# Kernel tuning notes

Measured on AMD Instinct MI355X. Metric: run time of the kernel, lower is better.

The kernel has to match this reference:

```python
import jax, jax.numpy as jnp
import numpy as np

# ---- static config (mirrors build() with the chosen init_kwargs) ----
B, H, W, C = 16, 56, 56, 128
KH, KW = 3, 3          # filter_size
SH, SW = 1, 1          # stride
NF = 256               # n_filters
IN_FEAT = C * KH * KW  # 1152
NNZ = int(1 * 0.2 * IN_FEAT * NF)  # multiple * density * n_parameters = 58982


def _make_indices():
    """Replicates the full='output' sparsity-pattern construction from build()."""
    rng = np.random.default_rng(0)
    per_col = NNZ // NF
    remain = NNZ % NF
    remain_cols = set(rng.choice(NF, remain, replace=False).tolist())
    chunks = []
    for col in rng.permutation(NF):
        k = per_col + (1 if int(col) in remain_cols else 0)
        rows = rng.choice(IN_FEAT, k, replace=False)
        chunks.append(np.stack([rows, np.full(k, col, dtype=np.int64)], axis=1))
    return np.concatenate(chunks, axis=0).astype(np.int32)  # (NNZ, 2) [row, col]


def setup_inputs() -> dict:
    key = jax.random.key(0)
    k1, k2 = jax.random.split(key)
    x = jax.random.normal(k1, (B, H, W, C), dtype=jnp.float32)
    limit = float(np.sqrt(6.0 / (IN_FEAT + NF)))  # glorot_uniform on the sparse values
    kernel = jax.random.uniform(k2, (NNZ,), jnp.float32, -limit, limit)
    bias = jnp.zeros((NF,), jnp.float32)
    indices = jnp.asarray(_make_indices())
    return {"x": x, "kernel": kernel, "bias": bias, "indices": indices}


def _im2col_valid(x):
    # tf.image.extract_patches ordering: patch positions row-major (di, dj),
    # channels fastest -> concatenate C-channel slices in (di, dj) order.
    oh = (H - KH) // SH + 1
    ow = (W - KW) // SW + 1
    cols = [x[:, di:di + oh * SH:SH, dj:dj + ow * SW:SW, :]
            for di in range(KH) for dj in range(KW)]
    return jnp.concatenate(cols, axis=-1), oh, ow  # (B, oh, ow, IN_FEAT)


def reference(x, kernel, bias, indices):
    patches, oh, ow = _im2col_valid(x)
    pm = patches.reshape(-1, IN_FEAT)  # (B*oh*ow, IN_FEAT)
    # Sparse (IN_FEAT, NF) weight: scatter values into a dense matrix
    # (indices are unique by construction, so .add == .set and is grad-safe).
    Wm = jnp.zeros((IN_FEAT, NF), dtype=pm.dtype).at[indices[:, 0], indices[:, 1]].add(kernel)
    out = pm @ Wm + bias            # sparse-dense matmul + bias
    out = jax.nn.relu(out)          # activation
    return out.reshape(B, oh, ow, NF)
```

## Files before the change

kernel.cpp:

```cpp
#include <hip/hip_runtime.h>

typedef unsigned short u16;
typedef __bf16 bf16x8 __attribute__((ext_vector_type(8)));
typedef float f32x4 __attribute__((ext_vector_type(4)));

#define B_   16
#define H_   56
#define W_   56
#define C_   128
#define OH_  54
#define OW_  54
#define NF_  256
#define KF_  1152
#define M_   46656
#define NNZ_ 58982

#define XB_ELEMS (B_*H_*W_*C_)
#define WT_ELEMS (KF_*NF_)

__device__ __forceinline__ u16 f2bf(float f) {
    unsigned u = __float_as_uint(f);
    u += 0x7FFFu + ((u >> 16) & 1u);
    return (u16)(u >> 16);
}

__device__ __forceinline__ void gload16(const void* g, void* l) {
    __builtin_amdgcn_global_load_lds(
        (const __attribute__((address_space(1))) unsigned int*)g,
        (__attribute__((address_space(3))) unsigned int*)l,
        16, 0, 0);
}

__global__ __launch_bounds__(256) void cvt_x_kernel(const float* __restrict__ x,
                                                    u16* __restrict__ xb,
                                                    u16* __restrict__ wt) {
    if (blockIdx.x < 144) {
        uint4 z = {0u, 0u, 0u, 0u};
        ((uint4*)wt)[blockIdx.x * 256 + threadIdx.x] = z;
    }
    int i = (blockIdx.x * 256 + threadIdx.x) * 8;
    float4 v0 = *(const float4*)(x + i);
    float4 v1 = *(const float4*)(x + i + 4);
    union { u16 u[8]; uint4 v; } r;
    r.u[0] = f2bf(v0.x); r.u[1] = f2bf(v0.y); r.u[2] = f2bf(v0.z); r.u[3] = f2bf(v0.w);
    r.u[4] = f2bf(v1.x); r.u[5] = f2bf(v1.y); r.u[6] = f2bf(v1.z); r.u[7] = f2bf(v1.w);
    *(uint4*)(xb + i) = r.v;
}

__global__ __launch_bounds__(256) void scatter_kernel(const float* __restrict__ kv,
                                                      const int* __restrict__ idx,
                                                      u16* __restrict__ wt) {
    int t = blockIdx.x * 256 + threadIdx.x;
    if (t >= NNZ_) return;
    int k   = idx[2*t];
    int col = idx[2*t + 1];
    wt[(k >> 3) * 2048 + col * 8 + (k & 7)] = f2bf(kv[t]);
}

__global__ __launch_bounds__(512, 2) void spconv_gemm(const u16* __restrict__ xb,
                                                      const u16* __restrict__ wt,
                                                      const float* __restrict__ bias,
                                                      float* __restrict__ out) {
    __shared__ __align__(16) u16 As[2][12288];
    __shared__ __align__(16) u16 Bs[2][16384];

    const int t    = threadIdx.x;
    const int l    = t & 63;
    const int w    = t >> 6;
    const int r16  = l & 15;
    const int ks   = l >> 4;
    const int wr   = w >> 2;
    const int wc   = w & 3;
    const int m0   = blockIdx.x * 192;

    const int r0  = t >> 3;
    const int sd  = t & 7;
    const int kco = (sd ^ (r0 & 7)) * 8;
    const u16* a_base[3];
#pragma unroll
    for (int j = 0; j < 3; ++j) {
        int mg  = m0 + r0 + j * 64;
        int bb  = mg / (OH_ * OW_);
        int rem = mg % (OH_ * OW_);
        int ii  = rem / OW_;
        int jj  = rem % OW_;
        a_base[j] = xb + ((bb * H_ + ii) * W_ + jj) * C_;
    }

    f32x4 acc[6][4];
    const f32x4 zz = {0.f, 0.f, 0.f, 0.f};
#pragma unroll
    for (int i = 0; i < 6; ++i)
#pragma unroll
        for (int j = 0; j < 4; ++j) acc[i][j] = zz;

#define ISSUE(kt, bi) do {                                                  \
    int g_  = (kt) >> 1;                                                    \
    int di_ = (g_ * 11) >> 5;                                               \
    int dj_ = g_ - 3 * di_;                                                 \
    int apix_ = (di_ * W_ + dj_) * C_ + ((kt) & 1) * 64 + kco;              \
    gload16(a_base[0] + apix_, &As[bi][t * 8]);                             \
    gload16(a_base[1] + apix_, &As[bi][t * 8 + 4096]);                      \
    gload16(a_base[2] + apix_, &As[bi][t * 8 + 8192]);                      \
    const u16* bsrc_ = wt + (kt) * 16384 + t * 8;                           \
    gload16(bsrc_,         &Bs[bi][t * 8]);                                 \
    gload16(bsrc_ + 4096,  &Bs[bi][t * 8 + 4096]);                          \
    gload16(bsrc_ + 8192,  &Bs[bi][t * 8 + 8192]);                          \
    gload16(bsrc_ + 12288, &Bs[bi][t * 8 + 12288]);                         \
} while (0)

#define COMPUTE(bi) do {                                                    \
    _Pragma("unroll")                                                       \
    for (int h = 0; h < 2; ++h) {                                           \
        const int chs_ = ((h * 4 + ks) ^ (r16 & 7)) * 8;                    \
        bf16x8 af_[6];                                                      \
        _Pragma("unroll")                                                   \
        for (int mf = 0; mf < 6; ++mf)                                      \
            af_[mf] = *(const bf16x8*)(&As[bi][(wr * 96 + mf * 16 + r16) * 64 + chs_]); \
        _Pragma("unroll")                                                   \
        for (int nf = 0; nf < 4; ++nf) {                                    \
            bf16x8 bf_ = *(const bf16x8*)(&Bs[bi][((h * 4 + ks) * 256 + wc * 64 + nf * 16 + r16) * 8]); \
            _Pragma("unroll")                                               \
            for (int mf = 0; mf < 6; ++mf)                                  \
                acc[mf][nf] = __builtin_amdgcn_mfma_f32_16x16x32_bf16(      \
                    af_[mf], bf_, acc[mf][nf], 0, 0, 0);                    \
        }                                                                   \
    }                                                                       \
} while (0)

#define WAITVM(n) asm volatile("s_waitcnt vmcnt(" #n ")" ::: "memory")
#define BAR() do { __builtin_amdgcn_s_barrier();                            \
                   asm volatile("" ::: "memory"); } while (0)

    ISSUE(0, 0);
    ISSUE(1, 1);

#pragma unroll
    for (int k = 0; k < 16; ++k) {
        WAITVM(7);
        BAR();
        COMPUTE(k & 1);
        BAR();
        ISSUE(k + 2, k & 1);
    }
    WAITVM(7); BAR(); COMPUTE(0);
    WAITVM(0); BAR(); COMPUTE(1);

#undef ISSUE
#undef COMPUTE
#undef WAITVM
#undef BAR

#pragma unroll
    for (int nf = 0; nf < 4; ++nf) {
        int col  = wc * 64 + nf * 16 + r16;
        float bv = bias[col];
#pragma unroll
        for (int mf = 0; mf < 6; ++mf) {
#pragma unroll
            for (int rr = 0; rr < 4; ++rr) {
                int row = m0 + wr * 96 + mf * 16 + ks * 4 + rr;
                float v = acc[mf][nf][rr] + bv;
                out[row * NF_ + col] = fmaxf(v, 0.f);
            }
        }
    }
}

extern "C" void kernel_launch(void* const* d_in, const int* in_sizes, int n_in,
                              void* d_out, int out_size, void* d_ws, size_t ws_size,
                              hipStream_t stream) {
    const float* x    = (const float*)d_in[0];
    const float* kv   = (const float*)d_in[1];
    const float* bias = (const float*)d_in[2];
    const int*   idx  = (const int*)d_in[3];
    float* out = (float*)d_out;

    u16* xb  = (u16*)d_ws;
    u16* wtp = (u16*)((char*)d_ws + (size_t)XB_ELEMS * 2);

    cvt_x_kernel<<<XB_ELEMS / (256 * 8), 256, 0, stream>>>(x, xb, wtp);
    scatter_kernel<<<(NNZ_ + 255) / 256, 256, 0, stream>>>(kv, idx, wtp);
    spconv_gemm<<<M_ / 192, 512, 0, stream>>>(xb, wtp, bias, out);
}
```

Measured before the change: 50.32 us.

## Interleave global loads with MFMA phases and remap blocks across XCDs

The GEMM main loop changes from whole-tile load then compute to a four-phase schedule per K step. Each phase reads LDS fragments, issues part of the next tile's global-to-LDS loads, and then runs 12 MFMAs under raised s_setprio with sched_barrier fences, so memory traffic overlaps tensor work. Block IDs are remapped so consecutive M tiles land on the same XCD, which should improve L2 reuse of overlapping im2col input rows. The occupancy hint in launch_bounds is dropped, and the many added barriers per step could add sync overhead.

```diff
diff --git a/kernel.cpp b/kernel.cpp
--- a/kernel.cpp
+++ b/kernel.cpp
@@ -57,10 +57,10 @@
     wt[(k >> 3) * 2048 + col * 8 + (k & 7)] = f2bf(kv[t]);
 }
 
-__global__ __launch_bounds__(512, 2) void spconv_gemm(const u16* __restrict__ xb,
-                                                      const u16* __restrict__ wt,
-                                                      const float* __restrict__ bias,
-                                                      float* __restrict__ out) {
+__global__ __launch_bounds__(512) void spconv_gemm(const u16* __restrict__ xb,
+                                                   const u16* __restrict__ wt,
+                                                   const float* __restrict__ bias,
+                                                   float* __restrict__ out) {
     __shared__ __align__(16) u16 As[2][12288];
     __shared__ __align__(16) u16 Bs[2][16384];
 
@@ -71,7 +71,12 @@
     const int ks   = l >> 4;
     const int wr   = w >> 2;
     const int wc   = w & 3;
-    const int m0   = blockIdx.x * 192;
+
+    const int nwg = gridDim.x;
+    const int q = nwg >> 3, rr_ = nwg & 7;
+    const int xcd = blockIdx.x & 7, inner = blockIdx.x >> 3;
+    const int wg = (xcd < rr_ ? xcd * (q + 1) : rr_ * (q + 1) + (xcd - rr_) * q) + inner;
+    const int m0 = wg * 192;
 
     const int r0  = t >> 3;
     const int sd  = t & 7;
@@ -94,62 +99,100 @@
 #pragma unroll
         for (int j = 0; j < 4; ++j) acc[i][j] = zz;
 
-#define ISSUE(kt, bi) do {                                                  \
-    int g_  = (kt) >> 1;                                                    \
+#define RA_(bi,h,mf) (*(const bf16x8*)(&As[bi][(wr * 96 + (mf) * 16 + r16) * 64 + (((h) * 4 + ks) ^ (r16 & 7)) * 8]))
+#define RB_(bi,h,nf) (*(const bf16x8*)(&Bs[bi][(((h) * 4 + ks) * 256 + wc * 64 + (nf) * 16 + r16) * 8]))
+
+#define IA_(kn,bj,j) do {                                                   \
+    int g_  = (kn) >> 1;                                                    \
     int di_ = (g_ * 11) >> 5;                                               \
     int dj_ = g_ - 3 * di_;                                                 \
-    int apix_ = (di_ * W_ + dj_) * C_ + ((kt) & 1) * 64 + kco;              \
-    gload16(a_base[0] + apix_, &As[bi][t * 8]);                             \
-    gload16(a_base[1] + apix_, &As[bi][t * 8 + 4096]);                      \
-    gload16(a_base[2] + apix_, &As[bi][t * 8 + 8192]);                      \
-    const u16* bsrc_ = wt + (kt) * 16384 + t * 8;                           \
-    gload16(bsrc_,         &Bs[bi][t * 8]);                                 \
-    gload16(bsrc_ + 4096,  &Bs[bi][t * 8 + 4096]);                          \
-    gload16(bsrc_ + 8192,  &Bs[bi][t * 8 + 8192]);                          \
-    gload16(bsrc_ + 12288, &Bs[bi][t * 8 + 12288]);                         \
+    gload16(a_base[j] + (di_ * W_ + dj_) * C_ + ((kn) & 1) * 64 + kco,      \
+            &As[bj][t * 8 + (j) * 4096]);                                   \
 } while (0)
-
-#define COMPUTE(bi) do {                                                    \
-    _Pragma("unroll")                                                       \
-    for (int h = 0; h < 2; ++h) {                                           \
-        const int chs_ = ((h * 4 + ks) ^ (r16 & 7)) * 8;                    \
-        bf16x8 af_[6];                                                      \
-        _Pragma("unroll")                                                   \
-        for (int mf = 0; mf < 6; ++mf)                                      \
-            af_[mf] = *(const bf16x8*)(&As[bi][(wr * 96 + mf * 16 + r16) * 64 + chs_]); \
-        _Pragma("unroll")                                                   \
-        for (int nf = 0; nf < 4; ++nf) {                                    \
-            bf16x8 bf_ = *(const bf16x8*)(&Bs[bi][((h * 4 + ks) * 256 + wc * 64 + nf * 16 + r16) * 8]); \
-            _Pragma("unroll")                                               \
-            for (int mf = 0; mf < 6; ++mf)                                  \
-                acc[mf][nf] = __builtin_amdgcn_mfma_f32_16x16x32_bf16(      \
-                    af_[mf], bf_, acc[mf][nf], 0, 0, 0);                    \
-        }                                                                   \
+#define IB_(kn,bj,j) gload16(wt + (kn) * 16384 + (j) * 4096 + t * 8,        \
+                             &Bs[bj][t * 8 + (j) * 4096])
+
+#define WAITVM(n) asm volatile("s_waitcnt vmcnt(" #n ")" ::: "memory")
+#define LG0()     asm volatile("s_waitcnt lgkmcnt(0)" ::: "memory")
+#define SB0()     __builtin_amdgcn_sched_barrier(0)
+#define BAR()     do { __builtin_amdgcn_s_barrier();                        \
+                       asm volatile("" ::: "memory"); } while (0)
+
+#define MM12(A0,A1,A2,MB,B0,B1,B2,B3) do {                                  \
+    acc[(MB)+0][0] = __builtin_amdgcn_mfma_f32_16x16x32_bf16(A0, B0, acc[(MB)+0][0], 0, 0, 0); \
+    acc[(MB)+1][0] = __builtin_amdgcn_mfma_f32_16x16x32_bf16(A1, B0, acc[(MB)+1][0], 0, 0, 0); \
+    acc[(MB)+2][0] = __builtin_amdgcn_mfma_f32_16x16x32_bf16(A2, B0, acc[(MB)+2][0], 0, 0, 0); \
+    acc[(MB)+0][1] = __builtin_amdgcn_mfma_f32_16x16x32_bf16(A0, B1, acc[(MB)+0][1], 0, 0, 0); \
+    acc[(MB)+1][1] = __builtin_amdgcn_mfma_f32_16x16x32_bf16(A1, B1, acc[(MB)+1][1], 0, 0, 0); \
+    acc[(MB)+2][1] = __builtin_amdgcn_mfma_f32_16x16x32_bf16(A2, B1, acc[(MB)+2][1], 0, 0, 0); \
+    acc[(MB)+0][2] = __builtin_amdgcn_mfma_f32_16x16x32_bf16(A0, B2, acc[(MB)+0][2], 0, 0, 0); \
+    acc[(MB)+1][2] = __builtin_amdgcn_mfma_f32_16x16x32_bf16(A1, B2, acc[(MB)+1][2], 0, 0, 0); \
+    acc[(MB)+2][2] = __builtin_amdgcn_mfma_f32_16x16x32_bf16(A2, B2, acc[(MB)+2][2], 0, 0, 0); \
+    acc[(MB)+0][3] = __builtin_amdgcn_mfma_f32_16x16x32_bf16(A0, B3, acc[(MB)+0][3], 0, 0, 0); \
+    acc[(MB)+1][3] = __builtin_amdgcn_mfma_f32_16x16x32_bf16(A1, B3, acc[(MB)+1][3], 0, 0, 0); \
+    acc[(MB)+2][3] = __builtin_amdgcn_mfma_f32_16x16x32_bf16(A2, B3, acc[(MB)+2][3], 0, 0, 0); \
+} while (0)
+
+#define SP(n) __builtin_amdgcn_s_setprio(n)
+
+#define STEP(bi_, kn_, DOISS, P2W) do {                                     \
+    const int bj_ = (bi_) ^ 1;                                              \
+                                                      \
+    WAITVM(2); BAR();                                                       \
+    {                                                                       \
+    bf16x8 bf0 = RB_(bi_,0,0), bf1 = RB_(bi_,0,1),                          \
+           bf2 = RB_(bi_,0,2), bf3 = RB_(bi_,0,3);                          \
+    bf16x8 a0 = RA_(bi_,0,0), a1 = RA_(bi_,0,1), a2 = RA_(bi_,0,2);         \
+    if (DOISS) { IA_(kn_, bj_, 0); IA_(kn_, bj_, 1); }                      \
+    BAR(); LG0(); SB0();                                                    \
+    SP(1); MM12(a0, a1, a2, 0, bf0, bf1, bf2, bf3); SP(0);                  \
+                                                      \
+    BAR();                                                                  \
+    bf16x8 a3 = RA_(bi_,0,3), a4 = RA_(bi_,0,4), a5 = RA_(bi_,0,5);         \
+    if (DOISS) { IA_(kn_, bj_, 2); IB_(kn_, bj_, 0); }                      \
+    BAR(); LG0(); SB0();                                                    \
+    SP(1); MM12(a3, a4, a5, 3, bf0, bf1, bf2, bf3); SP(0);                  \
+    }                                                                       \
+                                                      \
+    WAITVM(P2W); BAR();                                                     \
+    {                                                                       \
+    bf16x8 bf0 = RB_(bi_,1,0), bf1 = RB_(bi_,1,1),                          \
+           bf2 = RB_(bi_,1,2), bf3 = RB_(bi_,1,3);                          \
+    bf16x8 a0 = RA_(bi_,1,0), a1 = RA_(bi_,1,1), a2 = RA_(bi_,1,2);         \
+    if (DOISS) { IB_(kn_, bj_, 1); IB_(kn_, bj_, 2); }                      \
+    BAR(); LG0(); SB0();                                                    \
+    SP(1); MM12(a0, a1, a2, 0, bf0, bf1, bf2, bf3); SP(0);                  \
+                                                      \
+    BAR();                                                                  \
+    bf16x8 a3 = RA_(bi_,1,3), a4 = RA_(bi_,1,4), a5 = RA_(bi_,1,5);         \
+    if (DOISS) { IB_(kn_, bj_, 3); }                                        \
+    BAR(); LG0(); SB0();                                                    \
+    SP(1); MM12(a3, a4, a5, 3, bf0, bf1, bf2, bf3); SP(0);                  \
     }                                                                       \
 } while (0)
 
-#define WAITVM(n) asm volatile("s_waitcnt vmcnt(" #n ")" ::: "memory")
-#define BAR() do { __builtin_amdgcn_s_barrier();                            \
-                   asm volatile("" ::: "memory"); } while (0)
-
-    ISSUE(0, 0);
-    ISSUE(1, 1);
-
-#pragma unroll
-    for (int k = 0; k < 16; ++k) {
-        WAITVM(7);
-        BAR();
-        COMPUTE(k & 1);
-        BAR();
-        ISSUE(k + 2, k & 1);
-    }
-    WAITVM(7); BAR(); COMPUTE(0);
-    WAITVM(0); BAR(); COMPUTE(1);
-
-#undef ISSUE
-#undef COMPUTE
+    IA_(0, 0, 0); IA_(0, 0, 1); IA_(0, 0, 2);
+    IB_(0, 0, 0); IB_(0, 0, 1); IB_(0, 0, 2); IB_(0, 0, 3);
+
+#pragma unroll
+    for (int k = 0; k < 16; k += 2) {
+        STEP(0, k + 1, 1, 4);
+        STEP(1, k + 2, 1, 4);
+    }
+    STEP(0, 17, 1, 4);
+    STEP(1, 18, 0, 0);
+
+#undef RA_
+#undef RB_
+#undef IA_
+#undef IB_
 #undef WAITVM
+#undef LG0
+#undef SB0
 #undef BAR
+#undef MM12
+#undef SP
+#undef STEP
 
 #pragma unroll
     for (int nf = 0; nf < 4; ++nf) {
@@ -158,9 +201,9 @@
 #pragma unroll
         for (int mf = 0; mf < 6; ++mf) {
 #pragma unroll
-            for (int rr = 0; rr < 4; ++rr) {
-                int row = m0 + wr * 96 + mf * 16 + ks * 4 + rr;
-                float v = acc[mf][nf][rr] + bv;
+            for (int rg = 0; rg < 4; ++rg) {
+                int row = m0 + wr * 96 + mf * 16 + ks * 4 + rg;
+                float v = acc[mf][nf][rg] + bv;
                 out[row * NF_ + col] = fmaxf(v, 0.f);
             }
         }
```

Result: faster. 47.46 us (-5.7%).

## Use triple-buffered K=32 pipeline with split A/B loaders and XCD-aware block remap

Applied to the files above, without the earlier changes.

The GEMM main loop changes from a double-buffered K=64 stage to a triple-buffered K=32 stage. Half the threads load A and the other half load B, each with its own vmcnt wait, and the next stage is issued before compute so loads overlap more. Blocks are remapped so consecutive M tiles land on the same XCD for L2 locality, the LDS swizzle is adapted to the narrower tile, and launch_bounds no longer requests 2 blocks per CU. Each stage now does half the MFMA work but still pays two barriers, so sync overhead per FLOP doubles and occupancy may fall.

```diff
diff --git a/kernel.cpp b/kernel.cpp
--- a/kernel.cpp
+++ b/kernel.cpp
@@ -57,12 +57,12 @@
     wt[(k >> 3) * 2048 + col * 8 + (k & 7)] = f2bf(kv[t]);
 }
 
-__global__ __launch_bounds__(512, 2) void spconv_gemm(const u16* __restrict__ xb,
-                                                      const u16* __restrict__ wt,
-                                                      const float* __restrict__ bias,
-                                                      float* __restrict__ out) {
-    __shared__ __align__(16) u16 As[2][12288];
-    __shared__ __align__(16) u16 Bs[2][16384];
+__global__ __launch_bounds__(512) void spconv_gemm(const u16* __restrict__ xb,
+                                                   const u16* __restrict__ wt,
+                                                   const float* __restrict__ bias,
+                                                   float* __restrict__ out) {
+    __shared__ __align__(16) u16 As[3][192 * 4 * 8];
+    __shared__ __align__(16) u16 Bs[3][4 * 256 * 8];
 
     const int t    = threadIdx.x;
     const int l    = t & 63;
@@ -71,11 +71,16 @@
     const int ks   = l >> 4;
     const int wr   = w >> 2;
     const int wc   = w & 3;
-    const int m0   = blockIdx.x * 192;
 
-    const int r0  = t >> 3;
-    const int sd  = t & 7;
-    const int kco = (sd ^ (r0 & 7)) * 8;
+    const int nwg = gridDim.x;
+    const int q = nwg >> 3, rr_ = nwg & 7;
+    const int xcd = blockIdx.x & 7, inner = blockIdx.x >> 3;
+    const int wg = (xcd < rr_ ? xcd * (q + 1) : rr_ * (q + 1) + (xcd - rr_) * q) + inner;
+    const int m0 = wg * 192;
+
+    const int ua  = t & 255;
+    const int r0  = ua >> 2;
+    const int kco = (((ua & 3) ^ (r0 & 3) ^ ((r0 >> 2) & 3))) * 8;
     const u16* a_base[3];
 #pragma unroll
     for (int j = 0; j < 3; ++j) {
@@ -94,41 +99,46 @@
 #pragma unroll
         for (int j = 0; j < 4; ++j) acc[i][j] = zz;
 
+    const int cidx = ks ^ (r16 & 3) ^ ((r16 >> 2) & 3);
+
 #define ISSUE(kt, bi) do {                                                  \
-    int g_  = (kt) >> 1;                                                    \
-    int di_ = (g_ * 11) >> 5;                                               \
-    int dj_ = g_ - 3 * di_;                                                 \
-    int apix_ = (di_ * W_ + dj_) * C_ + ((kt) & 1) * 64 + kco;              \
-    gload16(a_base[0] + apix_, &As[bi][t * 8]);                             \
-    gload16(a_base[1] + apix_, &As[bi][t * 8 + 4096]);                      \
-    gload16(a_base[2] + apix_, &As[bi][t * 8 + 8192]);                      \
-    const u16* bsrc_ = wt + (kt) * 16384 + t * 8;                           \
-    gload16(bsrc_,         &Bs[bi][t * 8]);                                 \
-    gload16(bsrc_ + 4096,  &Bs[bi][t * 8 + 4096]);                          \
-    gload16(bsrc_ + 8192,  &Bs[bi][t * 8 + 8192]);                          \
-    gload16(bsrc_ + 12288, &Bs[bi][t * 8 + 12288]);                         \
+    if (t < 256) {                                                          \
+        int g_  = (kt) >> 2;                                                \
+        int di_ = (g_ * 11) >> 5;                                           \
+        int dj_ = g_ - 3 * di_;                                             \
+        int aoff_ = (di_ * W_ + dj_) * C_ + ((kt) & 3) * 32 + kco;          \
+        gload16(a_base[0] + aoff_, &As[bi][t * 8]);                         \
+        gload16(a_base[1] + aoff_, &As[bi][(t + 256) * 8]);                 \
+        gload16(a_base[2] + aoff_, &As[bi][(t + 512) * 8]);                 \
+    } else {                                                                \
+        const u16* bsrc_ = wt + (kt) * 8192 + (t - 256) * 8;                \
+        gload16(bsrc_,        &Bs[bi][(t - 256) * 8]);                      \
+        gload16(bsrc_ + 2048, &Bs[bi][(t - 256) * 8 + 2048]);               \
+        gload16(bsrc_ + 4096, &Bs[bi][(t - 256) * 8 + 4096]);               \
+        gload16(bsrc_ + 6144, &Bs[bi][(t - 256) * 8 + 6144]);               \
+    }                                                                       \
 } while (0)
 
 #define COMPUTE(bi) do {                                                    \
+    bf16x8 bfr_[4];                                                         \
     _Pragma("unroll")                                                       \
-    for (int h = 0; h < 2; ++h) {                                           \
-        const int chs_ = ((h * 4 + ks) ^ (r16 & 7)) * 8;                    \
-        bf16x8 af_[6];                                                      \
-        _Pragma("unroll")                                                   \
-        for (int mf = 0; mf < 6; ++mf)                                      \
-            af_[mf] = *(const bf16x8*)(&As[bi][(wr * 96 + mf * 16 + r16) * 64 + chs_]); \
-        _Pragma("unroll")                                                   \
-        for (int nf = 0; nf < 4; ++nf) {                                    \
-            bf16x8 bf_ = *(const bf16x8*)(&Bs[bi][((h * 4 + ks) * 256 + wc * 64 + nf * 16 + r16) * 8]); \
-            _Pragma("unroll")                                               \
-            for (int mf = 0; mf < 6; ++mf)                                  \
-                acc[mf][nf] = __builtin_amdgcn_mfma_f32_16x16x32_bf16(      \
-                    af_[mf], bf_, acc[mf][nf], 0, 0, 0);                    \
-        }                                                                   \
+    for (int nf = 0; nf < 4; ++nf)                                          \
+        bfr_[nf] = *(const bf16x8*)(&Bs[bi][(ks * 256 + wc * 64 + nf * 16 + r16) * 8]); \
+    _Pragma("unroll")                                                       \
+    for (int mf = 0; mf < 6; ++mf) {                                        \
+        int row_ = wr * 96 + mf * 16 + r16;                                 \
+        bf16x8 af_ = *(const bf16x8*)(&As[bi][(row_ * 4 + cidx) * 8]);      \
+        acc[mf][0] = __builtin_amdgcn_mfma_f32_16x16x32_bf16(af_, bfr_[0], acc[mf][0], 0, 0, 0); \
+        acc[mf][1] = __builtin_amdgcn_mfma_f32_16x16x32_bf16(af_, bfr_[1], acc[mf][1], 0, 0, 0); \
+        acc[mf][2] = __builtin_amdgcn_mfma_f32_16x16x32_bf16(af_, bfr_[2], acc[mf][2], 0, 0, 0); \
+        acc[mf][3] = __builtin_amdgcn_mfma_f32_16x16x32_bf16(af_, bfr_[3], acc[mf][3], 0, 0, 0); \
     }                                                                       \
 } while (0)
 
-#define WAITVM(n) asm volatile("s_waitcnt vmcnt(" #n ")" ::: "memory")
+#define WAITVM(na, nb) do {                                                 \
+    if (t < 256) { asm volatile("s_waitcnt vmcnt(" #na ")" ::: "memory"); } \
+    else         { asm volatile("s_waitcnt vmcnt(" #nb ")" ::: "memory"); } \
+} while (0)
 #define BAR() do { __builtin_amdgcn_s_barrier();                            \
                    asm volatile("" ::: "memory"); } while (0)
 
@@ -136,15 +146,18 @@
     ISSUE(1, 1);
 
 #pragma unroll
-    for (int k = 0; k < 16; ++k) {
-        WAITVM(7);
-        BAR();
-        COMPUTE(k & 1);
-        BAR();
-        ISSUE(k + 2, k & 1);
+    for (int k3 = 0; k3 < 11; ++k3) {
+        int k = 3 * k3;
+        WAITVM(3, 4); BAR(); ISSUE(k + 2, (k + 2) % 3); COMPUTE(0); BAR();
+        WAITVM(3, 4); BAR(); ISSUE(k + 3, (k + 3) % 3); COMPUTE(1); BAR();
+        if (k3 < 10) {
+            WAITVM(3, 4); BAR(); ISSUE(k + 4, (k + 4) % 3); COMPUTE(2); BAR();
+        }
     }
-    WAITVM(7); BAR(); COMPUTE(0);
-    WAITVM(0); BAR(); COMPUTE(1);
+    WAITVM(3, 4); BAR(); ISSUE(34, 1); COMPUTE(2); BAR();
+    WAITVM(3, 4); BAR(); ISSUE(35, 2); COMPUTE(0); BAR();
+    WAITVM(3, 4); BAR(); COMPUTE(1); BAR();
+    WAITVM(0, 0); BAR(); COMPUTE(2);
 
 #undef ISSUE
 #undef COMPUTE
@@ -158,9 +171,9 @@
 #pragma unroll
         for (int mf = 0; mf < 6; ++mf) {
 #pragma unroll
-            for (int rr = 0; rr < 4; ++rr) {
-                int row = m0 + wr * 96 + mf * 16 + ks * 4 + rr;
-                float v = acc[mf][nf][rr] + bv;
+            for (int rg = 0; rg < 4; ++rg) {
+                int row = m0 + wr * 96 + mf * 16 + ks * 4 + rg;
+                float v = acc[mf][nf][rg] + bv;
                 out[row * NF_ + col] = fmaxf(v, 0.f);
             }
         }
```

Measured after the change: 47.60 us. 5.4% less time.
